# Performance work log

Measured on AMD Instinct MI355X. Metric: run time of the kernel, lower is better.

The kernel has to match this reference:

```python
import jax, jax.numpy as jnp
import numpy as np

NUM_NODES = 10000
NUM_EDGES = 640000
IN_CH = 128
HID = 128
OUT_CH = 1


def setup_inputs() -> dict:
    key = jax.random.key(0)
    ks = jax.random.split(key, 12)
    x = jax.random.normal(ks[0], (NUM_NODES, IN_CH), dtype=jnp.float32)
    edge_index = jax.random.randint(ks[1], (2, NUM_EDGES), 0, NUM_NODES, dtype=jnp.int64)
    edge_weight = jax.random.uniform(ks[2], (NUM_EDGES,), dtype=jnp.float32)
    s1 = 1.0 / np.sqrt(IN_CH)
    s2 = 1.0 / np.sqrt(HID)
    W1 = jax.random.uniform(ks[3], (HID, IN_CH), minval=-s1, maxval=s1, dtype=jnp.float32)
    b1 = jnp.zeros((HID,), dtype=jnp.float32)
    W2 = jax.random.uniform(ks[4], (HID, HID), minval=-s2, maxval=s2, dtype=jnp.float32)
    b2 = jnp.zeros((HID,), dtype=jnp.float32)
    sc = 1.0 / np.sqrt(HID * 3)
    conv_w = jax.random.uniform(ks[5], (HID, HID, 3), minval=-sc, maxval=sc, dtype=jnp.float32)
    conv_b = jax.random.uniform(ks[6], (HID,), minval=-sc, maxval=sc, dtype=jnp.float32)
    fc_w = jax.random.uniform(ks[7], (OUT_CH, HID), minval=-s2, maxval=s2, dtype=jnp.float32)
    fc_b = jax.random.uniform(ks[8], (OUT_CH,), minval=-s2, maxval=s2, dtype=jnp.float32)
    return {"x": x, "edge_index": edge_index, "edge_weight": edge_weight,
            "W1": W1, "b1": b1, "W2": W2, "b2": b2,
            "conv_w": conv_w, "conv_b": conv_b, "fc_w": fc_w, "fc_b": fc_b}


def _gcn_conv(x, row, col, norm, W, b):
    # PyG GCNConv: linear (no bias in lin), normalized scatter-add, then bias
    xw = x @ W.T                                   # [N, out]
    msg = xw[row] * norm[:, None]                  # gather + edge scale [E, out]
    out = jax.ops.segment_sum(msg, col, num_segments=NUM_NODES)
    return out + b


def reference(x, edge_index, edge_weight, W1, b1, W2, b2, conv_w, conv_b, fc_w, fc_b):
    # gcn_norm with self-loops (fill_value=1.0)
    loop = jnp.arange(NUM_NODES, dtype=edge_index.dtype)
    row = jnp.concatenate([edge_index[0], loop])
    col = jnp.concatenate([edge_index[1], loop])
    w = jnp.concatenate([edge_weight, jnp.ones((NUM_NODES,), dtype=edge_weight.dtype)])
    deg = jax.ops.segment_sum(w, col, num_segments=NUM_NODES)
    dinv = jnp.where(deg > 0, jax.lax.rsqrt(deg), 0.0)
    norm = dinv[row] * w * dinv[col]

    h = jax.nn.relu(_gcn_conv(x, row, col, norm, W1, b1))
    # dropout is identity in eval mode
    h = jax.nn.relu(_gcn_conv(h, row, col, norm, W2, b2))

    # temporal conv1d over node axis: [N,H] -> [1,H,N]
    hc = h.T[None, :, :]
    hc = jax.lax.conv_general_dilated(hc, conv_w, window_strides=(1,),
                                      padding='SAME',
                                      dimension_numbers=('NCH', 'OIH', 'NCH'))
    hc = hc + conv_b[None, :, None]
    h = hc[0].T                                    # [N, H]

    return (h @ fc_w.T + fc_b).squeeze()           # [N]
```

## Files before the change

kernel.cpp:

```cpp
#include <hip/hip_runtime.h>
#include <hip/hip_bf16.h>

#define N_NODES 10000
#define N_EDGES 640000
#define CH 128
#define NB 64
#define EPB (N_EDGES / NB)
#define NCHUNK 40
#define NPAD 10240

__global__ __launch_bounds__(256) void fused_hist_gemm(const int* __restrict__ ei,
        const float* __restrict__ ew,
        const float* __restrict__ x, const float* __restrict__ W1,
        int* __restrict__ hist, float* __restrict__ dhist, int* __restrict__ pcs,
        float* __restrict__ out,
        const float* __restrict__ conv_w, const float* __restrict__ conv_b,
        const float* __restrict__ fc_w, const float* __restrict__ fc_b,
        float* __restrict__ vbuf, float* __restrict__ c0) {
    __shared__ __align__(16) char smem[NPAD * 8];
    int t = threadIdx.x;
    int bid = blockIdx.x;
    if (bid < NB) {
        int* h = (int*)smem;
        float* hf = (float*)(smem + NPAD * 4);
        for (int i = t; i < 2 * NPAD; i += 256) ((int*)smem)[i] = 0;
        __syncthreads();
        int e0 = bid * EPB;
        for (int i = t; i < EPB; i += 256) {
            int e = e0 + i;
            int c = ei[N_EDGES + e];
            atomicAdd(&h[c], 1);
            atomicAdd(&hf[c], ew[e]);
        }
        __syncthreads();
        for (int i = t; i < N_NODES; i += 256) {
            hist[bid * N_NODES + i] = h[i];
            dhist[bid * N_NODES + i] = hf[i];
        }
        int lane = t & 63, wave = t >> 6;
        for (int cch = wave; cch < NCHUNK; cch += 4) {
            int s = h[cch * 256 + lane] + h[cch * 256 + lane + 64]
                  + h[cch * 256 + lane + 128] + h[cch * 256 + lane + 192];
            #pragma unroll
            for (int off = 32; off > 0; off >>= 1) s += __shfl_down(s, off, 64);
            if (lane == 0) pcs[cch * NB + bid] = s;
        }
        return;
    }
    if (bid == NB + (N_NODES + 63) / 64) {
        for (int i = t; i <= 384; i += 256) {
            if (i < 384) {
                float s = 0.0f;
                for (int o = 0; o < CH; ++o) s += fc_w[o] * conv_w[o * 384 + i];
                vbuf[i] = s;
            } else {
                float s = fc_b[0];
                for (int o = 0; o < CH; ++o) s += fc_w[o] * conv_b[o];
                *c0 = s;
            }
        }
        return;
    }
    float (*As)[68]  = (float(*)[68])smem;
    float (*Ws)[132] = (float(*)[132])(smem + 32 * 68 * sizeof(float));
    int tx = t & 31;
    int ty = t >> 5;
    int row0 = (bid - NB) * 64;
    float acc[8][4] = {};
    for (int k0 = 0; k0 < 128; k0 += 32) {
        #pragma unroll
        for (int i = 0; i < 8; ++i) {
            int idx = t + i * 256;
            int r = idx >> 5, k = idx & 31;
            int gr = row0 + r;
            As[k][r] = (gr < N_NODES) ? x[gr * CH + k0 + k] : 0.0f;
        }
        #pragma unroll
        for (int i = 0; i < 16; ++i) {
            int idx = t + i * 256;
            int o = idx >> 5, k = idx & 31;
            Ws[k][o] = W1[o * CH + k0 + k];
        }
        __syncthreads();
        #pragma unroll
        for (int kk = 0; kk < 32; ++kk) {
            float a[8], w[4];
            #pragma unroll
            for (int j = 0; j < 8; ++j) a[j] = As[kk][ty * 8 + j];
            #pragma unroll
            for (int c = 0; c < 4; ++c) w[c] = Ws[kk][tx * 4 + c];
            #pragma unroll
            for (int j = 0; j < 8; ++j)
                #pragma unroll
                for (int c = 0; c < 4; ++c)
                    acc[j][c] += a[j] * w[c];
        }
        __syncthreads();
    }
    #pragma unroll
    for (int j = 0; j < 8; ++j) {
        int gr = row0 + ty * 8 + j;
        if (gr < N_NODES) {
            float4 v = make_float4(acc[j][0], acc[j][1], acc[j][2], acc[j][3]);
            *reinterpret_cast<float4*>(&out[gr * CH + tx * 4]) = v;
        }
    }
}

__global__ __launch_bounds__(256) void bofs_kernel(int* __restrict__ hist,
        const float* __restrict__ dhist, const int* __restrict__ pcs,
        int* __restrict__ tot, int* __restrict__ offs, float* __restrict__ dinv) {
    __shared__ int wred[4];
    __shared__ int wsum[4];
    __shared__ int base_sh;
    int blk = blockIdx.x, t = threadIdx.x;
    int lane = t & 63, wave = t >> 6;
    int bsum = 0;
    for (int i = t; i < blk * NB; i += 256) bsum += pcs[i];
    #pragma unroll
    for (int off = 32; off > 0; off >>= 1) bsum += __shfl_down(bsum, off, 64);
    if (lane == 0) wred[wave] = bsum;
    __syncthreads();
    if (t == 0) base_sh = wred[0] + wred[1] + wred[2] + wred[3];
    int n = blk * 256 + t;
    int v = 0;
    if (n < N_NODES) {
        float dsum = 0.0f;
        #pragma unroll 8
        for (int b = 0; b < NB; ++b) {
            v += hist[b * N_NODES + n];
            dsum += dhist[b * N_NODES + n];
        }
        tot[n] = v;
        dinv[n] = rsqrtf(dsum + 1.0f);
    }
    int s = v;
    #pragma unroll
    for (int off = 1; off < 64; off <<= 1) {
        int u = __shfl_up(s, off, 64);
        if (lane >= off) s += u;
    }
    if (lane == 63) wsum[wave] = s;
    __syncthreads();
    int wbase = 0;
    for (int i = 0; i < wave; ++i) wbase += wsum[i];
    if (n < N_NODES) {
        int run = base_sh + wbase + s - v;
        offs[n] = run;
        for (int b = 0; b < NB; ++b) {
            int h = hist[b * N_NODES + n];
            hist[b * N_NODES + n] = run;
            run += h;
        }
    }
}

__global__ __launch_bounds__(256) void scatter_kernel(const int* __restrict__ ei,
        const float* __restrict__ ew, const float* __restrict__ dinv,
        const int* __restrict__ bofs, int2* __restrict__ erec) {
    __shared__ int cur[N_NODES];
    __shared__ float di[N_NODES];
    int b = blockIdx.x, t = threadIdx.x;
    for (int i = t; i < N_NODES; i += 256) {
        cur[i] = bofs[b * N_NODES + i];
        di[i] = dinv[i];
    }
    __syncthreads();
    int e0 = b * EPB;
    for (int i = t; i < EPB; i += 256) {
        int e = e0 + i;
        int r = ei[e];
        int c = ei[N_EDGES + e];
        float v = di[r] * ew[e] * di[c];
        int p = atomicAdd(&cur[c], 1);
        erec[p] = make_int2(r, __float_as_int(v));
    }
}

__global__ __launch_bounds__(256) void regroup_kernel(const int2* __restrict__ erec,
        const int* __restrict__ offs, const int* __restrict__ cnt,
        int2* __restrict__ erec2) {
    __shared__ int curs[8][5];
    int g = threadIdx.x >> 5;
    int l = threadIdx.x & 31;
    int n = blockIdx.x * 8 + g;
    int start = offs[n];
    int num = cnt[n];
    int c0 = 0, c1 = 0, c2 = 0, c3 = 0;
    for (int i = l; i < num; i += 32) {
        int tl = erec[start + i].x >> 11;
        c0 += (tl == 0); c1 += (tl == 1); c2 += (tl == 2); c3 += (tl == 3);
    }
    #pragma unroll
    for (int off = 16; off > 0; off >>= 1) {
        c0 += __shfl_down(c0, off, 32);
        c1 += __shfl_down(c1, off, 32);
        c2 += __shfl_down(c2, off, 32);
        c3 += __shfl_down(c3, off, 32);
    }
    if (l == 0) {
        curs[g][0] = start;
        curs[g][1] = start + c0;
        curs[g][2] = start + c0 + c1;
        curs[g][3] = start + c0 + c1 + c2;
        curs[g][4] = start + c0 + c1 + c2 + c3;
    }
    __syncthreads();
    for (int i = l; i < num; i += 32) {
        int2 rec = erec[start + i];
        int tl = rec.x >> 11;
        int p = atomicAdd(&curs[g][tl], 1);
        erec2[p] = rec;
    }
}

__global__ __launch_bounds__(256) void agg_gemm_kernel(const float4* __restrict__ xw4,
        const int2* __restrict__ erec, const int* __restrict__ offs,
        const int* __restrict__ cnt, const float* __restrict__ dinv,
        const float4* __restrict__ bias4, const float* __restrict__ W2,
        float* __restrict__ out) {
    __shared__ float hs[8][128];
    int l = threadIdx.x & 31;
    int g = threadIdx.x >> 5;
    int n = blockIdx.x * 8 + g;
    float d = dinv[n];
    float dd = d * d;
    float4 self = xw4[n * 32 + l];
    float4 acc = make_float4(dd * self.x, dd * self.y, dd * self.z, dd * self.w);
    int start = offs[n];
    int num = cnt[n];
    int i = 0;
    for (; i + 8 <= num; i += 8) {
        int2 r[8];
        #pragma unroll
        for (int j = 0; j < 8; ++j) r[j] = erec[start + i + j];
        float4 f[8];
        #pragma unroll
        for (int j = 0; j < 8; ++j) f[j] = xw4[r[j].x * 32 + l];
        #pragma unroll
        for (int j = 0; j < 8; ++j) {
            float v = __int_as_float(r[j].y);
            acc.x += v * f[j].x; acc.y += v * f[j].y;
            acc.z += v * f[j].z; acc.w += v * f[j].w;
        }
    }
    for (; i < num; ++i) {
        int2 r = erec[start + i];
        float4 f = xw4[r.x * 32 + l];
        float v = __int_as_float(r.y);
        acc.x += v * f.x; acc.y += v * f.y; acc.z += v * f.z; acc.w += v * f.w;
    }
    float4 bb = bias4[l];
    acc.x = fmaxf(acc.x + bb.x, 0.0f);
    acc.y = fmaxf(acc.y + bb.y, 0.0f);
    acc.z = fmaxf(acc.z + bb.z, 0.0f);
    acc.w = fmaxf(acc.w + bb.w, 0.0f);
    *reinterpret_cast<float4*>(&hs[g][4 * l]) = acc;
    __syncthreads();
    int o = threadIdx.x & 127;
    int rg = threadIdx.x >> 7;
    const float4* w4p = reinterpret_cast<const float4*>(&W2[o * CH]);
    const float4* h0p = reinterpret_cast<const float4*>(&hs[rg * 4 + 0][0]);
    const float4* h1p = reinterpret_cast<const float4*>(&hs[rg * 4 + 1][0]);
    const float4* h2p = reinterpret_cast<const float4*>(&hs[rg * 4 + 2][0]);
    const float4* h3p = reinterpret_cast<const float4*>(&hs[rg * 4 + 3][0]);
    float a0 = 0.0f, a1 = 0.0f, a2 = 0.0f, a3 = 0.0f;
    #pragma unroll 8
    for (int k4 = 0; k4 < 32; ++k4) {
        float4 w = w4p[k4];
        float4 h0 = h0p[k4], h1 = h1p[k4], h2 = h2p[k4], h3 = h3p[k4];
        a0 += w.x * h0.x + w.y * h0.y + w.z * h0.z + w.w * h0.w;
        a1 += w.x * h1.x + w.y * h1.y + w.z * h1.z + w.w * h1.w;
        a2 += w.x * h2.x + w.y * h2.y + w.z * h2.z + w.w * h2.w;
        a3 += w.x * h3.x + w.y * h3.y + w.z * h3.z + w.w * h3.w;
    }
    int nb = blockIdx.x * 8 + rg * 4;
    out[(nb + 0) * CH + o] = a0;
    out[(nb + 1) * CH + o] = a1;
    out[(nb + 2) * CH + o] = a2;
    out[(nb + 3) * CH + o] = a3;
}

__global__ __launch_bounds__(256) void agg_kernel(const float4* __restrict__ xw4,
        const int2* __restrict__ erec, const int* __restrict__ offs,
        const int* __restrict__ cnt, const float* __restrict__ dinv,
        const float4* __restrict__ bias4, float4* __restrict__ out4) {
    int l = threadIdx.x & 31;
    int g = threadIdx.x >> 5;
    int n = blockIdx.x * 8 + g;
    float d = dinv[n];
    float dd = d * d;
    float4 self = xw4[n * 32 + l];
    float4 acc = make_float4(dd * self.x, dd * self.y, dd * self.z, dd * self.w);
    int start = offs[n];
    int num = cnt[n];
    int i = 0;
    for (; i + 8 <= num; i += 8) {
        int2 r[8];
        #pragma unroll
        for (int j = 0; j < 8; ++j) r[j] = erec[start + i + j];
        float4 f[8];
        #pragma unroll
        for (int j = 0; j < 8; ++j) f[j] = xw4[r[j].x * 32 + l];
        #pragma unroll
        for (int j = 0; j < 8; ++j) {
            float v = __int_as_float(r[j].y);
            acc.x += v * f[j].x; acc.y += v * f[j].y;
            acc.z += v * f[j].z; acc.w += v * f[j].w;
        }
    }
    for (; i < num; ++i) {
        int2 r = erec[start + i];
        float4 f = xw4[r.x * 32 + l];
        float v = __int_as_float(r.y);
        acc.x += v * f.x; acc.y += v * f.y; acc.z += v * f.z; acc.w += v * f.w;
    }
    float4 bb = bias4[l];
    acc.x = fmaxf(acc.x + bb.x, 0.0f);
    acc.y = fmaxf(acc.y + bb.y, 0.0f);
    acc.z = fmaxf(acc.z + bb.z, 0.0f);
    acc.w = fmaxf(acc.w + bb.w, 0.0f);
    out4[n * 32 + l] = acc;
}

__global__ __launch_bounds__(256) void convfc_kernel(const float* __restrict__ h,
        const float* __restrict__ v, const float* __restrict__ c0,
        float* __restrict__ out, int N) {
    int n = blockIdx.x * 4 + (threadIdx.x >> 6);
    int l = threadIdx.x & 63;
    if (n >= N) return;
    const float* hn = h + n * CH;
    float v0a = v[l * 3 + 0],        v1a = v[l * 3 + 1],        v2a = v[l * 3 + 2];
    float v0b = v[(l + 64) * 3 + 0], v1b = v[(l + 64) * 3 + 1], v2b = v[(l + 64) * 3 + 2];
    float p = hn[l] * v1a + hn[l + 64] * v1b;
    if (n > 0)     p += hn[l - CH] * v0a + hn[l + 64 - CH] * v0b;
    if (n < N - 1) p += hn[l + CH] * v2a + hn[l + 64 + CH] * v2b;
    #pragma unroll
    for (int off = 32; off > 0; off >>= 1) p += __shfl_down(p, off, 64);
    if (l == 0) out[n] = p + *c0;
}

extern "C" void kernel_launch(void* const* d_in, const int* in_sizes, int n_in,
                              void* d_out, int out_size, void* d_ws, size_t ws_size,
                              hipStream_t stream) {
    const float* x       = (const float*)d_in[0];
    const int*   ei      = (const int*)d_in[1];
    const float* ew      = (const float*)d_in[2];
    const float* W1      = (const float*)d_in[3];
    const float* b1      = (const float*)d_in[4];
    const float* W2      = (const float*)d_in[5];
    const float* b2      = (const float*)d_in[6];
    const float* conv_w  = (const float*)d_in[7];
    const float* conv_b  = (const float*)d_in[8];
    const float* fc_w    = (const float*)d_in[9];
    const float* fc_b    = (const float*)d_in[10];
    float* out = (float*)d_out;

    float* bufA   = (float*)d_ws;
    float* bufB   = bufA + N_NODES * CH;
    int2*  erec   = (int2*)(bufB + N_NODES * CH);
    int2*  erec2  = erec + N_EDGES;
    int*   hist   = (int*)(erec2 + N_EDGES);
    float* dhist  = (float*)(hist + NB * N_NODES);
    int*   pcs    = (int*)(dhist + NB * N_NODES);
    int*   tot    = pcs + NCHUNK * NB;
    int*   offs   = tot + N_NODES;
    float* dinv   = (float*)(offs + N_NODES);
    float* vbuf   = dinv + N_NODES;
    float* c0     = vbuf + 384;

    const int gemm_grid = (N_NODES + 63) / 64;

    fused_hist_gemm<<<NB + gemm_grid + 1, 256, 0, stream>>>(ei, ew, x, W1,
            hist, dhist, pcs, bufA, conv_w, conv_b, fc_w, fc_b, vbuf, c0);
    bofs_kernel<<<NCHUNK, 256, 0, stream>>>(hist, dhist, pcs, tot, offs, dinv);
    scatter_kernel<<<NB, 256, 0, stream>>>(ei, ew, dinv, hist, erec);
    regroup_kernel<<<N_NODES / 8, 256, 0, stream>>>(erec, offs, tot, erec2);
    agg_gemm_kernel<<<N_NODES / 8, 256, 0, stream>>>((const float4*)bufA, erec2, offs,
            tot, dinv, (const float4*)b1, W2, bufB);
    agg_kernel<<<N_NODES / 8, 256, 0, stream>>>((const float4*)bufB, erec2, offs, tot,
                                                dinv, (const float4*)b2, (float4*)bufA);
    convfc_kernel<<<(N_NODES + 3) / 4, 256, 0, stream>>>(bufA, vbuf, c0, out, N_NODES);
}
```

Before: 211.4 us.

## Split each node's edge aggregation across four warps with shared-memory reduction

Both aggregation kernels now use 1024-thread blocks, with four 32-lane groups per node instead of one. The groups share the node's 8-edge batches round-robin, then combine their partial sums through shared memory before bias and ReLU. The fused W2 GEMM is remapped so each thread computes one output row per node. This raises memory-level parallelism for the gathers, at the cost of an extra shared-memory reduction, a block-wide sync, and load imbalance when degree is small (about 64 edges, so about 2 batches per group).

```diff
diff --git a/kernel.cpp b/kernel.cpp
--- a/kernel.cpp
+++ b/kernel.cpp
@@ -214,26 +214,33 @@
     }
 }
 
-__global__ __launch_bounds__(256) void agg_gemm_kernel(const float4* __restrict__ xw4,
+__global__ __launch_bounds__(1024, 8) void agg_gemm_kernel(const float4* __restrict__ xw4,
         const int2* __restrict__ erec, const int* __restrict__ offs,
         const int* __restrict__ cnt, const float* __restrict__ dinv,
         const float4* __restrict__ bias4, const float* __restrict__ W2,
         float* __restrict__ out) {
+    __shared__ float4 part[8][4][32];
     __shared__ float hs[8][128];
-    int l = threadIdx.x & 31;
-    int g = threadIdx.x >> 5;
+    int t = threadIdx.x;
+    int l = t & 31;
+    int q = (t >> 5) & 3;
+    int g = t >> 7;
     int n = blockIdx.x * 8 + g;
-    float d = dinv[n];
-    float dd = d * d;
-    float4 self = xw4[n * 32 + l];
-    float4 acc = make_float4(dd * self.x, dd * self.y, dd * self.z, dd * self.w);
     int start = offs[n];
     int num = cnt[n];
-    int i = 0;
-    for (; i + 8 <= num; i += 8) {
+    float4 acc = make_float4(0.0f, 0.0f, 0.0f, 0.0f);
+    if (q == 0) {
+        float d = dinv[n];
+        float dd = d * d;
+        float4 self = xw4[n * 32 + l];
+        acc = make_float4(dd * self.x, dd * self.y, dd * self.z, dd * self.w);
+    }
+    int nbat = num >> 3;
+    for (int b = q; b < nbat; b += 4) {
+        int s0 = start + b * 8;
         int2 r[8];
         #pragma unroll
-        for (int j = 0; j < 8; ++j) r[j] = erec[start + i + j];
+        for (int j = 0; j < 8; ++j) r[j] = erec[s0 + j];
         float4 f[8];
         #pragma unroll
         for (int j = 0; j < 8; ++j) f[j] = xw4[r[j].x * 32 + l];
@@ -244,61 +251,67 @@
             acc.z += v * f[j].z; acc.w += v * f[j].w;
         }
     }
-    for (; i < num; ++i) {
-        int2 r = erec[start + i];
-        float4 f = xw4[r.x * 32 + l];
-        float v = __int_as_float(r.y);
-        acc.x += v * f.x; acc.y += v * f.y; acc.z += v * f.z; acc.w += v * f.w;
-    }
-    float4 bb = bias4[l];
-    acc.x = fmaxf(acc.x + bb.x, 0.0f);
-    acc.y = fmaxf(acc.y + bb.y, 0.0f);
-    acc.z = fmaxf(acc.z + bb.z, 0.0f);
-    acc.w = fmaxf(acc.w + bb.w, 0.0f);
-    *reinterpret_cast<float4*>(&hs[g][4 * l]) = acc;
-    __syncthreads();
-    int o = threadIdx.x & 127;
-    int rg = threadIdx.x >> 7;
+    if (q == 0) {
+        for (int i = start + nbat * 8; i < start + num; ++i) {
+            int2 r = erec[i];
+            float4 f = xw4[r.x * 32 + l];
+            float v = __int_as_float(r.y);
+            acc.x += v * f.x; acc.y += v * f.y; acc.z += v * f.z; acc.w += v * f.w;
+        }
+    }
+    part[g][q][l] = acc;
+    __syncthreads();
+    if (q == 0) {
+        float4 a0 = part[g][0][l], a1 = part[g][1][l];
+        float4 a2 = part[g][2][l], a3 = part[g][3][l];
+        float4 bb = bias4[l];
+        float4 r;
+        r.x = fmaxf(a0.x + a1.x + a2.x + a3.x + bb.x, 0.0f);
+        r.y = fmaxf(a0.y + a1.y + a2.y + a3.y + bb.y, 0.0f);
+        r.z = fmaxf(a0.z + a1.z + a2.z + a3.z + bb.z, 0.0f);
+        r.w = fmaxf(a0.w + a1.w + a2.w + a3.w + bb.w, 0.0f);
+        *reinterpret_cast<float4*>(&hs[g][4 * l]) = r;
+    }
+    __syncthreads();
+    int o = t & 127;
+    int rw = t >> 7;
     const float4* w4p = reinterpret_cast<const float4*>(&W2[o * CH]);
-    const float4* h0p = reinterpret_cast<const float4*>(&hs[rg * 4 + 0][0]);
-    const float4* h1p = reinterpret_cast<const float4*>(&hs[rg * 4 + 1][0]);
-    const float4* h2p = reinterpret_cast<const float4*>(&hs[rg * 4 + 2][0]);
-    const float4* h3p = reinterpret_cast<const float4*>(&hs[rg * 4 + 3][0]);
-    float a0 = 0.0f, a1 = 0.0f, a2 = 0.0f, a3 = 0.0f;
+    const float4* hp  = reinterpret_cast<const float4*>(&hs[rw][0]);
+    float a = 0.0f;
     #pragma unroll 8
     for (int k4 = 0; k4 < 32; ++k4) {
         float4 w = w4p[k4];
-        float4 h0 = h0p[k4], h1 = h1p[k4], h2 = h2p[k4], h3 = h3p[k4];
-        a0 += w.x * h0.x + w.y * h0.y + w.z * h0.z + w.w * h0.w;
-        a1 += w.x * h1.x + w.y * h1.y + w.z * h1.z + w.w * h1.w;
-        a2 += w.x * h2.x + w.y * h2.y + w.z * h2.z + w.w * h2.w;
-        a3 += w.x * h3.x + w.y * h3.y + w.z * h3.z + w.w * h3.w;
-    }
-    int nb = blockIdx.x * 8 + rg * 4;
-    out[(nb + 0) * CH + o] = a0;
-    out[(nb + 1) * CH + o] = a1;
-    out[(nb + 2) * CH + o] = a2;
-    out[(nb + 3) * CH + o] = a3;
-}
-
-__global__ __launch_bounds__(256) void agg_kernel(const float4* __restrict__ xw4,
+        float4 h = hp[k4];
+        a += w.x * h.x + w.y * h.y + w.z * h.z + w.w * h.w;
+    }
+    out[(blockIdx.x * 8 + rw) * CH + o] = a;
+}
+
+__global__ __launch_bounds__(1024, 8) void agg_kernel(const float4* __restrict__ xw4,
         const int2* __restrict__ erec, const int* __restrict__ offs,
         const int* __restrict__ cnt, const float* __restrict__ dinv,
         const float4* __restrict__ bias4, float4* __restrict__ out4) {
-    int l = threadIdx.x & 31;
-    int g = threadIdx.x >> 5;
+    __shared__ float4 part[8][4][32];
+    int t = threadIdx.x;
+    int l = t & 31;
+    int q = (t >> 5) & 3;
+    int g = t >> 7;
     int n = blockIdx.x * 8 + g;
-    float d = dinv[n];
-    float dd = d * d;
-    float4 self = xw4[n * 32 + l];
-    float4 acc = make_float4(dd * self.x, dd * self.y, dd * self.z, dd * self.w);
     int start = offs[n];
     int num = cnt[n];
-    int i = 0;
-    for (; i + 8 <= num; i += 8) {
+    float4 acc = make_float4(0.0f, 0.0f, 0.0f, 0.0f);
+    if (q == 0) {
+        float d = dinv[n];
+        float dd = d * d;
+        float4 self = xw4[n * 32 + l];
+        acc = make_float4(dd * self.x, dd * self.y, dd * self.z, dd * self.w);
+    }
+    int nbat = num >> 3;
+    for (int b = q; b < nbat; b += 4) {
+        int s0 = start + b * 8;
         int2 r[8];
         #pragma unroll
-        for (int j = 0; j < 8; ++j) r[j] = erec[start + i + j];
+        for (int j = 0; j < 8; ++j) r[j] = erec[s0 + j];
         float4 f[8];
         #pragma unroll
         for (int j = 0; j < 8; ++j) f[j] = xw4[r[j].x * 32 + l];
@@ -309,18 +322,27 @@
             acc.z += v * f[j].z; acc.w += v * f[j].w;
         }
     }
-    for (; i < num; ++i) {
-        int2 r = erec[start + i];
-        float4 f = xw4[r.x * 32 + l];
-        float v = __int_as_float(r.y);
-        acc.x += v * f.x; acc.y += v * f.y; acc.z += v * f.z; acc.w += v * f.w;
-    }
-    float4 bb = bias4[l];
-    acc.x = fmaxf(acc.x + bb.x, 0.0f);
-    acc.y = fmaxf(acc.y + bb.y, 0.0f);
-    acc.z = fmaxf(acc.z + bb.z, 0.0f);
-    acc.w = fmaxf(acc.w + bb.w, 0.0f);
-    out4[n * 32 + l] = acc;
+    if (q == 0) {
+        for (int i = start + nbat * 8; i < start + num; ++i) {
+            int2 r = erec[i];
+            float4 f = xw4[r.x * 32 + l];
+            float v = __int_as_float(r.y);
+            acc.x += v * f.x; acc.y += v * f.y; acc.z += v * f.z; acc.w += v * f.w;
+        }
+    }
+    part[g][q][l] = acc;
+    __syncthreads();
+    if (q == 0) {
+        float4 a0 = part[g][0][l], a1 = part[g][1][l];
+        float4 a2 = part[g][2][l], a3 = part[g][3][l];
+        float4 bb = bias4[l];
+        float4 r;
+        r.x = fmaxf(a0.x + a1.x + a2.x + a3.x + bb.x, 0.0f);
+        r.y = fmaxf(a0.y + a1.y + a2.y + a3.y + bb.y, 0.0f);
+        r.z = fmaxf(a0.z + a1.z + a2.z + a3.z + bb.z, 0.0f);
+        r.w = fmaxf(a0.w + a1.w + a2.w + a3.w + bb.w, 0.0f);
+        out4[n * 32 + l] = r;
+    }
 }
 
 __global__ __launch_bounds__(256) void convfc_kernel(const float* __restrict__ h,
@@ -376,9 +398,9 @@
     bofs_kernel<<<NCHUNK, 256, 0, stream>>>(hist, dhist, pcs, tot, offs, dinv);
     scatter_kernel<<<NB, 256, 0, stream>>>(ei, ew, dinv, hist, erec);
     regroup_kernel<<<N_NODES / 8, 256, 0, stream>>>(erec, offs, tot, erec2);
-    agg_gemm_kernel<<<N_NODES / 8, 256, 0, stream>>>((const float4*)bufA, erec2, offs,
+    agg_gemm_kernel<<<N_NODES / 8, 1024, 0, stream>>>((const float4*)bufA, erec2, offs,
             tot, dinv, (const float4*)b1, W2, bufB);
-    agg_kernel<<<N_NODES / 8, 256, 0, stream>>>((const float4*)bufB, erec2, offs, tot,
-                                                dinv, (const float4*)b2, (float4*)bufA);
+    agg_kernel<<<N_NODES / 8, 1024, 0, stream>>>((const float4*)bufB, erec2, offs, tot,
+                                                 dinv, (const float4*)b2, (float4*)bufA);
     convfc_kernel<<<(N_NODES + 3) / 4, 256, 0, stream>>>(bufA, vbuf, c0, out, N_NODES);
 }
```

Result: slower. 271.3 us (+28.3%).
